# Kernel tuning notes

Hardware: AMD Instinct MI355X
Metric: run time of the kernel (lower is better)

The kernel has to match this reference:

```python
import jax, jax.numpy as jnp
import numpy as np

B, T, E, D = 8, 2048, 1024, 64  # batch, seq, embed_dim, head_dim

def setup_inputs() -> dict:
    key = jax.random.key(0)
    kx, kq, kk, kv = jax.random.split(key, 4)
    scale = 1.0 / np.sqrt(E)
    return {
        "x": jax.random.normal(kx, (B, T, E), dtype=jnp.float32),
        "Wq": jax.random.normal(kq, (E, D), dtype=jnp.float32) * scale,
        "Wk": jax.random.normal(kk, (E, D), dtype=jnp.float32) * scale,
        "Wv": jax.random.normal(kv, (E, D), dtype=jnp.float32) * scale,
    }

def reference(x, Wq, Wk, Wv):
    # single-head causal attention (dropout in eval mode = identity)
    q = jnp.einsum('bte,ed->btd', x, Wq)
    k = jnp.einsum('bte,ed->btd', x, Wk)
    v = jnp.einsum('bte,ed->btd', x, Wv)
    head_dim = q.shape[-1]
    wei = jnp.einsum('btd,bsd->bts', q, k) * (head_dim ** -0.5)  # [B,T,T]
    causal = jnp.tril(jnp.ones((wei.shape[1], wei.shape[2]), dtype=bool))
    wei = jnp.where(causal, wei, -jnp.inf)
    wei = jax.nn.softmax(wei, axis=-1)
    out = jnp.einsum('bts,bsd->btd', wei, v)  # [B,T,D]
    return out
```

## Files before the change

kernel.cpp:

```cpp
#include <hip/hip_runtime.h>
#include <hip/hip_bf16.h>
#include <cstdint>
#include <cstddef>

#define B_ 8
#define T_ 2048
#define E_ 1024
#define D_ 64

typedef __attribute__((ext_vector_type(8))) short bf16x8;
typedef __attribute__((ext_vector_type(4))) float f32x4;
typedef __attribute__((ext_vector_type(16))) float f32x16;
typedef __attribute__((ext_vector_type(4))) unsigned short u16x4;

#define QSCALE 0.1803368801111204f

__device__ __forceinline__ short f2bf(float f){
    __hip_bfloat16 h = __float2bfloat16(f);
    return *reinterpret_cast<short*>(&h);
}

__device__ __forceinline__ bf16x8 cvt8v(const f32x4 a, const f32x4 b){
    bf16x8 r;
    r[0]=f2bf(a[0]); r[1]=f2bf(a[1]); r[2]=f2bf(a[2]); r[3]=f2bf(a[3]);
    r[4]=f2bf(b[0]); r[5]=f2bf(b[1]); r[6]=f2bf(b[2]); r[7]=f2bf(b[3]);
    return r;
}

__global__ __launch_bounds__(256) void wconv_kernel(
    const float* __restrict__ Wq, const float* __restrict__ Wk,
    const float* __restrict__ Wv, __hip_bfloat16* __restrict__ Wfrag)
{
    const int g = blockIdx.x*256 + threadIdx.x;
    const int l = g & 63;
    const int ntg = (g >> 6) % 6;
    const int cg = g / 384;
    const int n = ntg*32 + (l & 31);
    const int m = n >> 6;
    const int ncol = n & 63;
    const float* W = (m==0) ? Wq : (m==1) ? Wk : Wv;
    const float sc = (m==0) ? QSCALE : 1.0f;
    const int k0 = cg*16 + (l>>5)*8;
    bf16x8 r;
    #pragma unroll
    for (int j=0;j<8;++j)
        r[j] = f2bf(W[(size_t)(k0+j)*64 + ncol] * sc);
    *reinterpret_cast<bf16x8*>(Wfrag + (size_t)g*8) = r;
}

__global__ __launch_bounds__(384, 3) void proj_kernel(
    const float* __restrict__ x, const __hip_bfloat16* __restrict__ Wfrag,
    __hip_bfloat16* __restrict__ Qfrag, __hip_bfloat16* __restrict__ Kfrag,
    __hip_bfloat16* __restrict__ Vfrag)
{
    __shared__ __align__(16) unsigned short xs[2][32*64];
    __shared__ float vtQ[32*65];
    __shared__ float vtK[32*65];
    __shared__ float vtV[32*65];
    const int tid = threadIdx.x;
    const int w = tid>>6, l = tid&63;
    const int l31 = l&31, kg = l>>5;
    const float* xp = x + (size_t)blockIdx.x*32*E_;

    f32x16 acc;
    #pragma unroll
    for (int j=0;j<16;++j) acc[j]=0.f;

    const bf16x8* Wfp = reinterpret_cast<const bf16x8*>(Wfrag);

    bf16x8 btA[4], btB[4];
    #pragma unroll
    for (int c=0;c<4;++c)
        btA[c] = Wfp[(size_t)(((0*4+c)*6 + w)*64 + l)];

    const int srow = tid>>3, sc8 = tid&7;

    if (tid < 256){
        f32x4 v0 = *reinterpret_cast<const f32x4*>(xp + (size_t)srow*E_ + sc8*8);
        f32x4 v1 = *reinterpret_cast<const f32x4*>(xp + (size_t)srow*E_ + sc8*8 + 4);
        *reinterpret_cast<bf16x8*>((char*)&xs[0][0] + srow*128 + ((sc8*16) ^ ((srow&7)<<4))) = cvt8v(v0, v1);
    }
    __syncthreads();

#define PSTEP(T, BC, BN)                                                       \
    {                                                                          \
        const int t = (T);                                                     \
        if (t+1 < 16){                                                         \
            _Pragma("unroll")                                                  \
            for (int c=0;c<4;++c)                                              \
                BN[c] = Wfp[(size_t)((((t+1)*4+c)*6 + w)*64 + l)];             \
        }                                                                      \
        f32x4 xa0, xa1;                                                        \
        if (t+1 < 16 && tid < 256){                                            \
            xa0 = *reinterpret_cast<const f32x4*>(xp + (size_t)srow*E_ + (t+1)*64 + sc8*8);     \
            xa1 = *reinterpret_cast<const f32x4*>(xp + (size_t)srow*E_ + (t+1)*64 + sc8*8 + 4); \
        }                                                                      \
        const char* xb = (const char*)&xs[t&1][0];                             \
        _Pragma("unroll")                                                      \
        for (int c=0;c<4;++c){                                                 \
            bf16x8 af = *reinterpret_cast<const bf16x8*>(xb + l31*128 + (((c*32 + kg*16)) ^ ((l31&7)<<4))); \
            acc = __builtin_amdgcn_mfma_f32_32x32x16_bf16(af, BC[c], acc, 0,0,0); \
        }                                                                      \
        if (t+1 < 16){                                                         \
            if (tid < 256)                                                     \
                *reinterpret_cast<bf16x8*>((char*)&xs[(t+1)&1][0] + srow*128 + ((sc8*16) ^ ((srow&7)<<4))) = cvt8v(xa0, xa1); \
            __syncthreads();                                                   \
        }                                                                      \
    }

    for (int t2=0; t2<8; ++t2){
        PSTEP(2*t2,   btA, btB)
        PSTEP(2*t2+1, btB, btA)
    }
#undef PSTEP

    {
        float* vtX = (w<2) ? vtQ : (w<4) ? vtK : vtV;
        const int col = (w&1)*32 + l31;
        #pragma unroll
        for (int reg=0; reg<16; ++reg){
            const int mr = (reg&3) + 8*(reg>>2) + 4*kg;
            vtX[mr*65 + col] = acc[reg];
        }
    }
    __syncthreads();
    if (tid < 256){
        const int q = blockIdx.x, b = q>>6, q63 = q&63, t = q63>>1;
        const int su  = (tid>>7)&1, ksw = (tid>>6)&1, lw = tid&63;
        const int lw15 = lw&15, lwg = lw>>4;
        {
            f32x4 a0, a1;
            #pragma unroll
            for (int j=0;j<4;++j) a0[j] = vtQ[(su*16+lw15)*65 + ksw*32 + lwg*8 + j];
            #pragma unroll
            for (int j=0;j<4;++j) a1[j] = vtQ[(su*16+lw15)*65 + ksw*32 + lwg*8 + 4 + j];
            const size_t gi = ((size_t)(b*128 + 2*q63 + su)*2 + ksw)*64 + lw;
            *reinterpret_cast<bf16x8*>(Qfrag + gi*8) = cvt8v(a0, a1);
        }
        {
            f32x4 a0, a1;
            #pragma unroll
            for (int j=0;j<4;++j) a0[j] = vtK[(su*16+lw15)*65 + ksw*32 + lwg*8 + j];
            #pragma unroll
            for (int j=0;j<4;++j) a1[j] = vtK[(su*16+lw15)*65 + ksw*32 + lwg*8 + 4 + j];
            const int nt = (q&1)*2 + su;
            const size_t gi = (((size_t)(b*32 + t)*4 + nt)*2 + ksw)*64 + lw;
            *reinterpret_cast<bf16x8*>(Kfrag + gi*8) = cvt8v(a0, a1);
        }
        {
            const int dt = tid>>6;
            bf16x8 pk;
            #pragma unroll
            for (int j=0;j<8;++j)
                pk[j] = f2bf(vtV[(lwg*8+j)*65 + dt*16 + lw15]);
            const size_t gi = (((size_t)(b*32 + t)*4 + dt)*2 + (q&1))*64 + lw;
            *reinterpret_cast<bf16x8*>(Vfrag + gi*8) = pk;
        }
    }
}

__global__ __launch_bounds__(256, 4) void fattn_kernel(
    const __hip_bfloat16* __restrict__ Qfrag, const __hip_bfloat16* __restrict__ Kfrag,
    const __hip_bfloat16* __restrict__ Vfrag, float* __restrict__ out)
{
    __shared__ __align__(16) unsigned short Pl[4][1024];
    __shared__ float Morg[4][16];
    __shared__ float Lorg[4][64];
    __shared__ __align__(16) float Oorg[4][16*64];

    const int tid = threadIdx.x;
    const int w = tid>>6, l = tid&63;
    const int l15 = l&15, lg = l>>4;

    const int b = blockIdx.x & 7;
    const int g = blockIdx.x >> 8;
    const int r = (blockIdx.x >> 3) & 31;
    const int s = (g==0) ? (127 - r) : (g==1) ? (64 + r) : (g==2) ? (63 - r) : r;
    const int n = (s>>2) + 1;
    const size_t batchoff = (size_t)b * T_ * 64;

    const bf16x8* qfp = reinterpret_cast<const bf16x8*>(Qfrag);
    const bf16x8* kfp = reinterpret_cast<const bf16x8*>(Kfrag);
    const bf16x8* vfp = reinterpret_cast<const bf16x8*>(Vfrag);
    char* pw = (char*)&Pl[w][0];

    const int qrow = s*16 + l15;
    const bf16x8 qf0 = qfp[(size_t)((b*128 + s)*2 + 0)*64 + l];
    const bf16x8 qf1 = qfp[(size_t)((b*128 + s)*2 + 1)*64 + l];

    f32x4 o[4];
    #pragma unroll
    for (int i=0;i<4;++i) o[i] = (f32x4){0.f,0.f,0.f,0.f};
    float mrun = -1e30f, lrun = 0.f;

    for (int kvt = w; kvt < n; kvt += 4){
        bf16x8 kf[8], vf[8];
        #pragma unroll
        for (int ks=0;ks<2;++ks)
            #pragma unroll
            for (int nt=0;nt<4;++nt){
                kf[ks*4+nt] = kfp[(size_t)(((b*32 + kvt)*4 + nt)*2 + ks)*64 + l];
                vf[ks*4+nt] = vfp[(size_t)(((b*32 + kvt)*4 + nt)*2 + ks)*64 + l];
            }
        f32x4 s4[4];
        #pragma unroll
        for (int nt=0;nt<4;++nt) s4[nt] = (f32x4){0.f,0.f,0.f,0.f};
        __builtin_amdgcn_s_setprio(1);
        #pragma unroll
        for (int ks=0;ks<2;++ks){
            const bf16x8 qf = ks ? qf1 : qf0;
            #pragma unroll
            for (int nt=0;nt<4;++nt)
                s4[nt] = __builtin_amdgcn_mfma_f32_16x16x32_bf16(kf[ks*4+nt], qf, s4[nt], 0,0,0);
        }
        __builtin_amdgcn_s_setprio(0);

        if (kvt == n-1){
            const int kv0 = kvt*64;
            #pragma unroll
            for (int nt=0;nt<4;++nt)
                #pragma unroll
                for (int rr=0;rr<4;++rr){
                    const int kv = kv0 + nt*16 + lg*4 + rr;
                    if (kv > qrow) s4[nt][rr] = -1e30f;
                }
        }

        float pmLoc;
        {
            float m0 = fmaxf(fmaxf(s4[0][0],s4[0][1]), fmaxf(s4[0][2],s4[0][3]));
            float m1 = fmaxf(fmaxf(s4[1][0],s4[1][1]), fmaxf(s4[1][2],s4[1][3]));
            float m2 = fmaxf(fmaxf(s4[2][0],s4[2][1]), fmaxf(s4[2][2],s4[2][3]));
            float m3 = fmaxf(fmaxf(s4[3][0],s4[3][1]), fmaxf(s4[3][2],s4[3][3]));
            pmLoc = fmaxf(fmaxf(m0,m1), fmaxf(m2,m3));
        }
        if (__any(pmLoc > mrun + 8.0f)){
            float pm = pmLoc;
            pm = fmaxf(pm, __shfl_xor(pm, 16));
            pm = fmaxf(pm, __shfl_xor(pm, 32));
            const float mn = fmaxf(mrun, pm);
            const float scl = exp2f(mrun - mn);
            mrun = mn; lrun *= scl;
            #pragma unroll
            for (int dt=0;dt<4;++dt)
                #pragma unroll
                for (int j=0;j<4;++j) o[dt][j] *= scl;
        }
        float rs = 0.f;
        #pragma unroll
        for (int nt=0;nt<4;++nt)
            #pragma unroll
            for (int rr=0;rr<4;++rr){
                const float pv = exp2f(s4[nt][rr] - mrun);
                s4[nt][rr] = pv; rs += pv;
            }
        lrun += rs;

        #pragma unroll
        for (int nt=0;nt<4;++nt){
            u16x4 pk;
            #pragma unroll
            for (int rr=0;rr<4;++rr) pk[rr] = (unsigned short)f2bf(s4[nt][rr]);
            *reinterpret_cast<u16x4*>(pw + l15*128 + ((nt*32 + lg*8) ^ ((l15&7)<<4))) = pk;
        }
        __builtin_amdgcn_s_setprio(1);
        #pragma unroll
        for (int ks=0;ks<2;++ks){
            bf16x8 pf = *reinterpret_cast<const bf16x8*>(pw + l15*128 + ((ks*64 + lg*16) ^ ((l15&7)<<4)));
            #pragma unroll
            for (int dt=0;dt<4;++dt)
                o[dt] = __builtin_amdgcn_mfma_f32_16x16x32_bf16(vf[ks*4+dt], pf, o[dt], 0,0,0);
        }
        __builtin_amdgcn_s_setprio(0);
    }

    #pragma unroll
    for (int dt=0;dt<4;++dt)
        *reinterpret_cast<f32x4*>(&Oorg[w][l15*64 + dt*16 + lg*4]) = o[dt];
    Lorg[w][l] = lrun;
    if (lg == 0) Morg[w][l15] = mrun;
    __syncthreads();
    {
        const int q = tid >> 4, dg = tid & 15;
        const float m0=Morg[0][q], m1=Morg[1][q], m2=Morg[2][q], m3=Morg[3][q];
        const float M = fmaxf(fmaxf(m0,m1), fmaxf(m2,m3));
        const float a0=exp2f(m0-M), a1=exp2f(m1-M), a2=exp2f(m2-M), a3=exp2f(m3-M);
        float L = 0.f;
        #pragma unroll
        for (int lgg=0; lgg<4; ++lgg){
            L += a0*Lorg[0][lgg*16+q] + a1*Lorg[1][lgg*16+q]
               + a2*Lorg[2][lgg*16+q] + a3*Lorg[3][lgg*16+q];
        }
        const float inv = 1.0f / L;
        float* op = out + batchoff + (size_t)(s*16 + q)*64 + dg*4;
        #pragma unroll
        for (int j=0;j<4;++j){
            const float v = a0*Oorg[0][q*64+dg*4+j] + a1*Oorg[1][q*64+dg*4+j]
                          + a2*Oorg[2][q*64+dg*4+j] + a3*Oorg[3][q*64+dg*4+j];
            op[j] = v * inv;
        }
    }
}

extern "C" void kernel_launch(void* const* d_in, const int* in_sizes, int n_in,
                              void* d_out, int out_size, void* d_ws, size_t ws_size,
                              hipStream_t stream) {
    const float* x  = (const float*)d_in[0];
    const float* Wq = (const float*)d_in[1];
    const float* Wk = (const float*)d_in[2];
    const float* Wv = (const float*)d_in[3];
    float* out = (float*)d_out;

    const size_t NTOK = (size_t)B_*T_*64;
    __hip_bfloat16* Wfrag = (__hip_bfloat16*)d_ws;
    __hip_bfloat16* Qfrag = Wfrag + (size_t)24576*8;
    __hip_bfloat16* Kfrag = Qfrag + NTOK;
    __hip_bfloat16* Vfrag = Kfrag + NTOK;

    wconv_kernel<<<96, 256, 0, stream>>>(Wq, Wk, Wv, Wfrag);
    proj_kernel<<<512, 384, 0, stream>>>(x, Wfrag, Qfrag, Kfrag, Vfrag);
    fattn_kernel<<<1024, 256, 0, stream>>>(Qfrag, Kfrag, Vfrag, out);
}
```

Baseline: 37.76 us.

## Process two 16-row query tiles per block to reuse K/V fragments

Each attention block now computes 32 query rows (two 16-row tiles) against the same loaded K/V fragments, halving the grid to 512 blocks. This targets redundant global loads of K and V across query tiles. In exchange, register pressure and shared memory rise, occupancy bounds drop from 4 to 2, and there are fewer blocks to balance the causal workload.

```diff
diff --git a/kernel.cpp b/kernel.cpp
--- a/kernel.cpp
+++ b/kernel.cpp
@@ -159,24 +159,24 @@
     }
 }
 
-__global__ __launch_bounds__(256, 4) void fattn_kernel(
+__global__ __launch_bounds__(256, 2) void fattn_kernel(
     const __hip_bfloat16* __restrict__ Qfrag, const __hip_bfloat16* __restrict__ Kfrag,
     const __hip_bfloat16* __restrict__ Vfrag, float* __restrict__ out)
 {
-    __shared__ __align__(16) unsigned short Pl[4][1024];
-    __shared__ float Morg[4][16];
-    __shared__ float Lorg[4][64];
-    __shared__ __align__(16) float Oorg[4][16*64];
+    __shared__ __align__(16) unsigned short Pl[4][2048];
+    __shared__ float Morg[4][2][16];
+    __shared__ float Lorg[4][2][64];
+    __shared__ __align__(16) float Oorg[4][2][16*64];
 
     const int tid = threadIdx.x;
     const int w = tid>>6, l = tid&63;
     const int l15 = l&15, lg = l>>4;
 
     const int b = blockIdx.x & 7;
+    const int r = (blockIdx.x >> 3) & 31;
     const int g = blockIdx.x >> 8;
-    const int r = (blockIdx.x >> 3) & 31;
-    const int s = (g==0) ? (127 - r) : (g==1) ? (64 + r) : (g==2) ? (63 - r) : r;
-    const int n = (s>>2) + 1;
+    const int s = g ? r : (63 - r);
+    const int n = (s>>1) + 1;
     const size_t batchoff = (size_t)b * T_ * 64;
 
     const bf16x8* qfp = reinterpret_cast<const bf16x8*>(Qfrag);
@@ -184,14 +184,17 @@
     const bf16x8* vfp = reinterpret_cast<const bf16x8*>(Vfrag);
     char* pw = (char*)&Pl[w][0];
 
-    const int qrow = s*16 + l15;
-    const bf16x8 qf0 = qfp[(size_t)((b*128 + s)*2 + 0)*64 + l];
-    const bf16x8 qf1 = qfp[(size_t)((b*128 + s)*2 + 1)*64 + l];
-
-    f32x4 o[4];
-    #pragma unroll
-    for (int i=0;i<4;++i) o[i] = (f32x4){0.f,0.f,0.f,0.f};
-    float mrun = -1e30f, lrun = 0.f;
+    const int qrow0 = s*32 + l15;
+    const int qrow1 = s*32 + 16 + l15;
+    const bf16x8 q00 = qfp[(size_t)((b*128 + 2*s  )*2 + 0)*64 + l];
+    const bf16x8 q01 = qfp[(size_t)((b*128 + 2*s  )*2 + 1)*64 + l];
+    const bf16x8 q10 = qfp[(size_t)((b*128 + 2*s+1)*2 + 0)*64 + l];
+    const bf16x8 q11 = qfp[(size_t)((b*128 + 2*s+1)*2 + 1)*64 + l];
+
+    f32x4 o0[4], o1[4];
+    #pragma unroll
+    for (int i=0;i<4;++i){ o0[i] = (f32x4){0.f,0.f,0.f,0.f}; o1[i] = (f32x4){0.f,0.f,0.f,0.f}; }
+    float m0run = -1e30f, l0run = 0.f, m1run = -1e30f, l1run = 0.f;
 
     for (int kvt = w; kvt < n; kvt += 4){
         bf16x8 kf[8], vf[8];
@@ -202,16 +205,21 @@
                 kf[ks*4+nt] = kfp[(size_t)(((b*32 + kvt)*4 + nt)*2 + ks)*64 + l];
                 vf[ks*4+nt] = vfp[(size_t)(((b*32 + kvt)*4 + nt)*2 + ks)*64 + l];
             }
-        f32x4 s4[4];
-        #pragma unroll
-        for (int nt=0;nt<4;++nt) s4[nt] = (f32x4){0.f,0.f,0.f,0.f};
+
+        f32x4 s40[4], s41[4];
+        #pragma unroll
+        for (int nt=0;nt<4;++nt){ s40[nt] = (f32x4){0.f,0.f,0.f,0.f}; s41[nt] = (f32x4){0.f,0.f,0.f,0.f}; }
         __builtin_amdgcn_s_setprio(1);
         #pragma unroll
         for (int ks=0;ks<2;++ks){
-            const bf16x8 qf = ks ? qf1 : qf0;
-            #pragma unroll
-            for (int nt=0;nt<4;++nt)
-                s4[nt] = __builtin_amdgcn_mfma_f32_16x16x32_bf16(kf[ks*4+nt], qf, s4[nt], 0,0,0);
+            const bf16x8 qa = ks ? q01 : q00;
+            const bf16x8 qb = ks ? q11 : q10;
+            #pragma unroll
+            for (int nt=0;nt<4;++nt)
+                s40[nt] = __builtin_amdgcn_mfma_f32_16x16x32_bf16(kf[ks*4+nt], qa, s40[nt], 0,0,0);
+            #pragma unroll
+            for (int nt=0;nt<4;++nt)
+                s41[nt] = __builtin_amdgcn_mfma_f32_16x16x32_bf16(kf[ks*4+nt], qb, s41[nt], 0,0,0);
         }
         __builtin_amdgcn_s_setprio(0);
 
@@ -222,81 +230,124 @@
                 #pragma unroll
                 for (int rr=0;rr<4;++rr){
                     const int kv = kv0 + nt*16 + lg*4 + rr;
-                    if (kv > qrow) s4[nt][rr] = -1e30f;
+                    if (kv > qrow0) s40[nt][rr] = -1e30f;
+                    if (kv > qrow1) s41[nt][rr] = -1e30f;
                 }
         }
 
-        float pmLoc;
-        {
-            float m0 = fmaxf(fmaxf(s4[0][0],s4[0][1]), fmaxf(s4[0][2],s4[0][3]));
-            float m1 = fmaxf(fmaxf(s4[1][0],s4[1][1]), fmaxf(s4[1][2],s4[1][3]));
-            float m2 = fmaxf(fmaxf(s4[2][0],s4[2][1]), fmaxf(s4[2][2],s4[2][3]));
-            float m3 = fmaxf(fmaxf(s4[3][0],s4[3][1]), fmaxf(s4[3][2],s4[3][3]));
-            pmLoc = fmaxf(fmaxf(m0,m1), fmaxf(m2,m3));
-        }
-        if (__any(pmLoc > mrun + 8.0f)){
-            float pm = pmLoc;
-            pm = fmaxf(pm, __shfl_xor(pm, 16));
-            pm = fmaxf(pm, __shfl_xor(pm, 32));
-            const float mn = fmaxf(mrun, pm);
-            const float scl = exp2f(mrun - mn);
-            mrun = mn; lrun *= scl;
+        {
+            float a0 = fmaxf(fmaxf(s40[0][0],s40[0][1]), fmaxf(s40[0][2],s40[0][3]));
+            float a1 = fmaxf(fmaxf(s40[1][0],s40[1][1]), fmaxf(s40[1][2],s40[1][3]));
+            float a2 = fmaxf(fmaxf(s40[2][0],s40[2][1]), fmaxf(s40[2][2],s40[2][3]));
+            float a3 = fmaxf(fmaxf(s40[3][0],s40[3][1]), fmaxf(s40[3][2],s40[3][3]));
+            float pmLoc = fmaxf(fmaxf(a0,a1), fmaxf(a2,a3));
+            if (__any(pmLoc > m0run + 8.0f)){
+                float pm = pmLoc;
+                pm = fmaxf(pm, __shfl_xor(pm, 16));
+                pm = fmaxf(pm, __shfl_xor(pm, 32));
+                const float mn = fmaxf(m0run, pm);
+                const float scl = exp2f(m0run - mn);
+                m0run = mn; l0run *= scl;
+                #pragma unroll
+                for (int dt=0;dt<4;++dt)
+                    #pragma unroll
+                    for (int j=0;j<4;++j) o0[dt][j] *= scl;
+            }
+            float rs = 0.f;
+            #pragma unroll
+            for (int nt=0;nt<4;++nt)
+                #pragma unroll
+                for (int rr=0;rr<4;++rr){
+                    const float pv = exp2f(s40[nt][rr] - m0run);
+                    s40[nt][rr] = pv; rs += pv;
+                }
+            l0run += rs;
+        }
+        {
+            float a0 = fmaxf(fmaxf(s41[0][0],s41[0][1]), fmaxf(s41[0][2],s41[0][3]));
+            float a1 = fmaxf(fmaxf(s41[1][0],s41[1][1]), fmaxf(s41[1][2],s41[1][3]));
+            float a2 = fmaxf(fmaxf(s41[2][0],s41[2][1]), fmaxf(s41[2][2],s41[2][3]));
+            float a3 = fmaxf(fmaxf(s41[3][0],s41[3][1]), fmaxf(s41[3][2],s41[3][3]));
+            float pmLoc = fmaxf(fmaxf(a0,a1), fmaxf(a2,a3));
+            if (__any(pmLoc > m1run + 8.0f)){
+                float pm = pmLoc;
+                pm = fmaxf(pm, __shfl_xor(pm, 16));
+                pm = fmaxf(pm, __shfl_xor(pm, 32));
+                const float mn = fmaxf(m1run, pm);
+                const float scl = exp2f(m1run - mn);
+                m1run = mn; l1run *= scl;
+                #pragma unroll
+                for (int dt=0;dt<4;++dt)
+                    #pragma unroll
+                    for (int j=0;j<4;++j) o1[dt][j] *= scl;
+            }
+            float rs = 0.f;
+            #pragma unroll
+            for (int nt=0;nt<4;++nt)
+                #pragma unroll
+                for (int rr=0;rr<4;++rr){
+                    const float pv = exp2f(s41[nt][rr] - m1run);
+                    s41[nt][rr] = pv; rs += pv;
+                }
+            l1run += rs;
+        }
+
+        #pragma unroll
+        for (int nt=0;nt<4;++nt){
+            u16x4 pk0, pk1;
+            #pragma unroll
+            for (int rr=0;rr<4;++rr){
+                pk0[rr] = (unsigned short)f2bf(s40[nt][rr]);
+                pk1[rr] = (unsigned short)f2bf(s41[nt][rr]);
+            }
+            *reinterpret_cast<u16x4*>(pw + l15*128 + ((nt*32 + lg*8) ^ ((l15&7)<<4))) = pk0;
+            *reinterpret_cast<u16x4*>(pw + 2048 + l15*128 + ((nt*32 + lg*8) ^ ((l15&7)<<4))) = pk1;
+        }
+
+        __builtin_amdgcn_s_setprio(1);
+        #pragma unroll
+        for (int ks=0;ks<2;++ks){
+            bf16x8 pf0 = *reinterpret_cast<const bf16x8*>(pw + l15*128 + ((ks*64 + lg*16) ^ ((l15&7)<<4)));
+            bf16x8 pf1 = *reinterpret_cast<const bf16x8*>(pw + 2048 + l15*128 + ((ks*64 + lg*16) ^ ((l15&7)<<4)));
             #pragma unroll
             for (int dt=0;dt<4;++dt)
-                #pragma unroll
-                for (int j=0;j<4;++j) o[dt][j] *= scl;
-        }
-        float rs = 0.f;
-        #pragma unroll
-        for (int nt=0;nt<4;++nt)
-            #pragma unroll
-            for (int rr=0;rr<4;++rr){
-                const float pv = exp2f(s4[nt][rr] - mrun);
-                s4[nt][rr] = pv; rs += pv;
-            }
-        lrun += rs;
-
-        #pragma unroll
-        for (int nt=0;nt<4;++nt){
-            u16x4 pk;
-            #pragma unroll
-            for (int rr=0;rr<4;++rr) pk[rr] = (unsigned short)f2bf(s4[nt][rr]);
-            *reinterpret_cast<u16x4*>(pw + l15*128 + ((nt*32 + lg*8) ^ ((l15&7)<<4))) = pk;
-        }
-        __builtin_amdgcn_s_setprio(1);
-        #pragma unroll
-        for (int ks=0;ks<2;++ks){
-            bf16x8 pf = *reinterpret_cast<const bf16x8*>(pw + l15*128 + ((ks*64 + lg*16) ^ ((l15&7)<<4)));
+                o0[dt] = __builtin_amdgcn_mfma_f32_16x16x32_bf16(vf[ks*4+dt], pf0, o0[dt], 0,0,0);
             #pragma unroll
             for (int dt=0;dt<4;++dt)
-                o[dt] = __builtin_amdgcn_mfma_f32_16x16x32_bf16(vf[ks*4+dt], pf, o[dt], 0,0,0);
+                o1[dt] = __builtin_amdgcn_mfma_f32_16x16x32_bf16(vf[ks*4+dt], pf1, o1[dt], 0,0,0);
         }
         __builtin_amdgcn_s_setprio(0);
     }
 
     #pragma unroll
-    for (int dt=0;dt<4;++dt)
-        *reinterpret_cast<f32x4*>(&Oorg[w][l15*64 + dt*16 + lg*4]) = o[dt];
-    Lorg[w][l] = lrun;
-    if (lg == 0) Morg[w][l15] = mrun;
+    for (int dt=0;dt<4;++dt){
+        *reinterpret_cast<f32x4*>(&Oorg[w][0][l15*64 + dt*16 + lg*4]) = o0[dt];
+        *reinterpret_cast<f32x4*>(&Oorg[w][1][l15*64 + dt*16 + lg*4]) = o1[dt];
+    }
+    Lorg[w][0][l] = l0run;
+    Lorg[w][1][l] = l1run;
+    if (lg == 0){
+        Morg[w][0][l15] = m0run;
+        Morg[w][1][l15] = m1run;
+    }
     __syncthreads();
     {
-        const int q = tid >> 4, dg = tid & 15;
-        const float m0=Morg[0][q], m1=Morg[1][q], m2=Morg[2][q], m3=Morg[3][q];
+        const int h = tid>>7, q = (tid>>3)&15, d0 = (tid&7)*8;
+        const float m0=Morg[0][h][q], m1=Morg[1][h][q], m2=Morg[2][h][q], m3=Morg[3][h][q];
         const float M = fmaxf(fmaxf(m0,m1), fmaxf(m2,m3));
         const float a0=exp2f(m0-M), a1=exp2f(m1-M), a2=exp2f(m2-M), a3=exp2f(m3-M);
         float L = 0.f;
         #pragma unroll
-        for (int lgg=0; lgg<4; ++lgg){
-            L += a0*Lorg[0][lgg*16+q] + a1*Lorg[1][lgg*16+q]
-               + a2*Lorg[2][lgg*16+q] + a3*Lorg[3][lgg*16+q];
+        for (int gg=0; gg<4; ++gg){
+            L += a0*Lorg[0][h][gg*16+q] + a1*Lorg[1][h][gg*16+q]
+               + a2*Lorg[2][h][gg*16+q] + a3*Lorg[3][h][gg*16+q];
         }
         const float inv = 1.0f / L;
-        float* op = out + batchoff + (size_t)(s*16 + q)*64 + dg*4;
-        #pragma unroll
-        for (int j=0;j<4;++j){
-            const float v = a0*Oorg[0][q*64+dg*4+j] + a1*Oorg[1][q*64+dg*4+j]
-                          + a2*Oorg[2][q*64+dg*4+j] + a3*Oorg[3][q*64+dg*4+j];
+        float* op = out + batchoff + (size_t)(s*32 + h*16 + q)*64 + d0;
+        #pragma unroll
+        for (int j=0;j<8;++j){
+            const float v = a0*Oorg[0][h][q*64+d0+j] + a1*Oorg[1][h][q*64+d0+j]
+                          + a2*Oorg[2][h][q*64+d0+j] + a3*Oorg[3][h][q*64+d0+j];
             op[j] = v * inv;
         }
     }
@@ -319,5 +370,5 @@
 
     wconv_kernel<<<96, 256, 0, stream>>>(Wq, Wk, Wv, Wfrag);
     proj_kernel<<<512, 384, 0, stream>>>(x, Wfrag, Qfrag, Kfrag, Vfrag);
-    fattn_kernel<<<1024, 256, 0, stream>>>(Qfrag, Kfrag, Vfrag, out);
-}
+    fattn_kernel<<<512, 256, 0, stream>>>(Qfrag, Kfrag, Vfrag, out);
+}
```

New measurement: 41.97 us. 11.1% more time.
